# Performance work log

Measured on AMD Instinct MI355X. Metric: run time of the kernel, lower is better.

## Reference

```python
import jax, jax.numpy as jnp
import numpy as np

S, D, BN, GH, AH, FCH = 18, 512, 32, 128, 16, 512


def setup_inputs() -> dict:
    key = jax.random.key(0)
    ks = jax.random.split(key, 20)
    B = 8192
    sc = 0.05
    inp = {
        "local_styles": jax.random.normal(ks[0], (B, S, D), jnp.float32),
        "global_styles": jax.random.normal(ks[1], (B, S, D), jnp.float32),
        "target_ages": jax.random.uniform(ks[2], (B,), jnp.float32),
        # per-style bottleneck MLPs (512->32->32), stacked over styles
        "bn_w1": jax.random.normal(ks[3], (S, D, BN), jnp.float32) * sc,
        "bn_b1": jnp.zeros((S, BN), jnp.float32),
        "bn_w2": jax.random.normal(ks[4], (S, BN, BN), jnp.float32) * sc,
        "bn_b2": jnp.zeros((S, BN), jnp.float32),
        # global mlp (18*32 -> 128 -> 128)
        "gm_w1": jax.random.normal(ks[5], (S * BN, GH), jnp.float32) * sc,
        "gm_b1": jnp.zeros((GH,), jnp.float32),
        "gm_w2": jax.random.normal(ks[6], (GH, GH), jnp.float32) * sc,
        "gm_b2": jnp.zeros((GH,), jnp.float32),
        # age mlp (1 -> 16 -> 16)
        "age_w1": jax.random.normal(ks[7], (1, AH), jnp.float32) * sc,
        "age_b1": jnp.zeros((AH,), jnp.float32),
        "age_w2": jax.random.normal(ks[8], (AH, AH), jnp.float32) * sc,
        "age_b2": jnp.zeros((AH,), jnp.float32),
        # per-style fc MLPs (128+16+512 -> 512 -> 512), stacked over styles
        "fc_w1": jax.random.normal(ks[9], (S, GH + AH + D, FCH), jnp.float32) * sc,
        "fc_b1": jnp.zeros((S, FCH), jnp.float32),
        "fc_w2": jax.random.normal(ks[10], (S, FCH, D), jnp.float32) * sc,
        "fc_b2": jnp.zeros((S, D), jnp.float32),
    }
    return inp


def reference(local_styles, global_styles, target_ages,
              bn_w1, bn_b1, bn_w2, bn_b2,
              gm_w1, gm_b1, gm_w2, gm_b2,
              age_w1, age_b1, age_w2, age_b2,
              fc_w1, fc_b1, fc_w2, fc_b2):
    B = global_styles.shape[0]
    # per-style bottlenecks as batched GEMMs over the style axis
    h = jax.nn.relu(jnp.einsum('bsd,sdk->bsk', global_styles, bn_w1) + bn_b1)
    h = jnp.einsum('bsk,skm->bsm', h, bn_w2) + bn_b2          # [B, S, 32]
    gf = h.reshape(B, S * BN)                                  # concat over styles
    gf = jax.nn.relu(gf @ gm_w1 + gm_b1) @ gm_w2 + gm_b2      # [B, 128]
    af = target_ages[:, None]                                  # [B, 1]
    af = jax.nn.relu(af @ age_w1 + age_b1) @ age_w2 + age_b2   # [B, 16]
    gfa = jnp.concatenate([gf, af], axis=1)                    # [B, 144]
    # per-style fc: input is [global_feats, style_i] -> [B, S, 656]
    x = jnp.concatenate([jnp.broadcast_to(gfa[:, None, :], (B, S, GH + AH)),
                         global_styles], axis=2)
    y = jax.nn.relu(jnp.einsum('bsf,sfh->bsh', x, fc_w1) + fc_b1)
    y = jnp.einsum('bsh,shd->bsd', y, fc_w2) + fc_b2
    return y + global_styles
```

## Files before the change

kernel.cpp:

```cpp
#include <hip/hip_runtime.h>

typedef unsigned short u16;
typedef unsigned int   u32;
typedef __attribute__((ext_vector_type(4))) float floatx4;
typedef __attribute__((ext_vector_type(8))) short shortx8;

#define BB 8192
#define SS 18
#define DD 512

__device__ __forceinline__ u16 f2bf(float f){
  u32 u = __float_as_uint(f);
  return (u16)((u + 0x7FFFu + ((u >> 16) & 1u)) >> 16);
}

__device__ __forceinline__ shortx8 pack8v(floatx4 a, floatx4 b){
  shortx8 t;
  t[0]=(short)f2bf(a[0]); t[1]=(short)f2bf(a[1]); t[2]=(short)f2bf(a[2]); t[3]=(short)f2bf(a[3]);
  t[4]=(short)f2bf(b[0]); t[5]=(short)f2bf(b[1]); t[6]=(short)f2bf(b[2]); t[7]=(short)f2bf(b[3]);
  return t;
}

__device__ __forceinline__ void gload16(const void* g, void* l){
  __builtin_amdgcn_global_load_lds((const __attribute__((address_space(1))) void*)g,
                                   (__attribute__((address_space(3))) void*)l, 16, 0, 0);
}

template<int CALLS>
__device__ __forceinline__ void gstage(const char* src, size_t rowStrideB, int chunkByteOff,
                                       char* lds, int wid, int lane){
#pragma unroll
  for (int i=0;i<CALLS;++i){
    int base = (wid*CALLS + i)*1024;
    int off  = base + lane*16;
    int row  = off >> 7;
    int blk  = ((off >> 4) & 7) ^ (row & 7);
    gload16(src + (size_t)row*rowStrideB + chunkByteOff + blk*16, lds + base);
  }
}

__device__ __forceinline__ void lds_store4(char* buf, int row, int rowBytes, int khByte,
                                           int swzMask, const shortx8* v){
#pragma unroll
  for (int q=0;q<4;++q){
    int off = row*rowBytes + khByte + q*16;
    off ^= (row & swzMask) << 4;
    *(shortx8*)(buf + off) = v[q];
  }
}

__device__ __forceinline__ void stage_bf16(char* buf, const u16* gsrc, size_t srcRowBytes, int tid){
  int row = tid >> 1, kh = tid & 1;
  const char* p = (const char*)gsrc + (size_t)row*srcRowBytes + kh*64;
  shortx8 v[4];
#pragma unroll
  for (int q=0;q<4;++q) v[q] = *(const shortx8*)(p + q*16);
  lds_store4(buf, row, 128, kh*64, 7, v);
}

__device__ __forceinline__ shortx8 lds_frag(const char* buf, int row, int rowBytes, int kByte,
                                            int swzMask, int lane){
  int off = row*rowBytes + kByte + ((lane>>4)<<4);
  off ^= (row & swzMask) << 4;
  return *(const shortx8*)(buf + off);
}

template<int MF, int NF>
__device__ __forceinline__ void mma64(const char* As, const char* Bs, int wm, int wn, int lane,
                                      floatx4 acc[MF][NF]){
#pragma unroll
  for (int kk=0; kk<2; ++kk){
    shortx8 a[MF], b[NF];
#pragma unroll
    for (int i=0;i<MF;++i) a[i] = lds_frag(As, wm + i*16 + (lane&15), 128, kk*64, 7, lane);
#pragma unroll
    for (int j=0;j<NF;++j) b[j] = lds_frag(Bs, wn + j*16 + (lane&15), 128, kk*64, 7, lane);
#pragma unroll
    for (int i=0;i<MF;++i)
#pragma unroll
      for (int j=0;j<NF;++j)
        acc[i][j] = __builtin_amdgcn_mfma_f32_16x16x32_bf16(a[i], b[j], acc[i][j], 0, 0, 0);
  }
}

__device__ __forceinline__ int xcd_swz(int bid, int nwg){
  int q = nwg >> 3;
  return (bid & 7)*q + (bid >> 3);
}

__global__ __launch_bounds__(256) void transpose_w2(const float* __restrict__ src,
                                                    u16* __restrict__ dst,
                                                    int sKstride, int kSrcOff, int Kuse,
                                                    int N, int Kpad, int kDstOff){
  __shared__ float tile[32][33];
  int s = blockIdx.z;
  int k0 = blockIdx.x*32, n0 = blockIdx.y*32;
  int tx = threadIdx.x & 31, ty = threadIdx.x >> 5;
#pragma unroll
  for (int r=0;r<4;++r){
    int k = k0 + ty*4 + r;
    float v = (k < Kuse) ? src[((size_t)s*sKstride + kSrcOff + k)*N + n0 + tx] : 0.f;
    tile[ty*4+r][tx] = v;
  }
  __syncthreads();
#pragma unroll
  for (int r=0;r<4;++r){
    int n = n0 + ty*4 + r;
    dst[((size_t)s*N + n)*Kpad + kDstOff + k0 + tx] = f2bf(tile[tx][ty*4+r]);
  }
}

__global__ __launch_bounds__(256) void k_bn(const float* __restrict__ gs,
     const u16* __restrict__ w1t, const u16* __restrict__ w2t,
     const float* __restrict__ b1, const float* __restrict__ b2,
     u16* __restrict__ h2b){
  __shared__ __align__(16) char SMB[40960];
  int tid = threadIdx.x, lane = tid & 63, wid = tid >> 6;
  int nb = xcd_swz(blockIdx.x, 1152);
  int m0 = (nb & 63)*128, s = nb >> 6;
  floatx4 acc[2][2] = {};
  const char*  Bsrc = (const char*)w1t + (size_t)s*32*1024;
  const float* Ags  = gs + ((size_t)(m0 + (tid>>1))*SS + s)*DD + (tid&1)*32;
  floatx4 fr[8];
  gstage<1>((const char*)Bsrc, 1024, 0, SMB+32768, wid, lane);
#pragma unroll
  for (int q=0;q<8;++q) fr[q] = *(const floatx4*)(Ags + q*4);
  for (int c=0;c<8;++c){
    char* Asc = SMB + (c&1)*16384;
    char* Bsc = SMB + 32768 + (c&1)*4096;
    { shortx8 v[4];
#pragma unroll
      for (int q=0;q<4;++q) v[q] = pack8v(fr[2*q], fr[2*q+1]);
      lds_store4(Asc, tid>>1, 128, (tid&1)*64, 7, v); }
    __syncthreads();
    int cn = c+1;
    if (cn < 8){
      gstage<1>(Bsrc, 1024, cn*128, SMB + 32768 + (cn&1)*4096, wid, lane);
      const float* p = Ags + cn*64;
#pragma unroll
      for (int q=0;q<8;++q) fr[q] = *(const floatx4*)(p + q*4);
    }
    mma64<2,2>(Asc, Bsc, wid*32, 0, lane, acc);
  }
  __syncthreads();
  char* G1  = SMB;
  char* W2s = SMB + 8192;
#pragma unroll
  for (int i=0;i<2;++i)
#pragma unroll
   for (int j=0;j<2;++j){
    int col = j*16 + (lane&15);
    float bias = b1[s*32 + col];
#pragma unroll
    for (int r=0;r<4;++r){
      int row = wid*32 + i*16 + ((lane>>4)<<2) + r;
      float v = fmaxf(acc[i][j][r] + bias, 0.f);
      int off = (row*64 + col*2) ^ ((row&3)<<4);
      *(u16*)(G1 + off) = f2bf(v);
    }
  }
  if (tid < 32){
    const u16* p = w2t + (size_t)s*32*32 + tid*32;
#pragma unroll
    for (int q=0;q<4;++q){
      int off = (tid*64 + q*16) ^ ((tid&3)<<4);
      *(shortx8*)(W2s + off) = *(const shortx8*)(p + q*8);
    }
  }
  __syncthreads();
  floatx4 acc2[2][2] = {};
  {
    shortx8 a[2], b[2];
#pragma unroll
    for (int i=0;i<2;++i) a[i] = lds_frag(G1,  wid*32 + i*16 + (lane&15), 64, 0, 3, lane);
#pragma unroll
    for (int j=0;j<2;++j) b[j] = lds_frag(W2s, j*16 + (lane&15),          64, 0, 3, lane);
#pragma unroll
    for (int i=0;i<2;++i)
#pragma unroll
      for (int j=0;j<2;++j)
        acc2[i][j] = __builtin_amdgcn_mfma_f32_16x16x32_bf16(a[i], b[j], acc2[i][j], 0,0,0);
  }
#pragma unroll
  for (int i=0;i<2;++i)
#pragma unroll
   for (int j=0;j<2;++j){
    int col = j*16 + (lane&15);
    float bias = b2[s*32 + col];
#pragma unroll
    for (int r=0;r<4;++r){
      int row = wid*32 + i*16 + ((lane>>4)<<2) + r;
      h2b[((size_t)(m0+row)*SS + s)*32 + col] = f2bf(acc2[i][j][r] + bias);
    }
  }
}

__global__ __launch_bounds__(256) void k_gm(const u16* __restrict__ h2b,
     const u16* __restrict__ w1t, const u16* __restrict__ w2t,
     const float* __restrict__ b1, const float* __restrict__ b2,
     const float* __restrict__ ta, const float* __restrict__ aw1, const float* __restrict__ ab1,
     const float* __restrict__ aw2, const float* __restrict__ ab2,
     u16* __restrict__ gfab){
  __shared__ __align__(16) char As[128*128];
  __shared__ __align__(16) char Bs[128*128];
  __shared__ __align__(16) char G1[128*256];
  int tid=threadIdx.x, lane=tid&63, w=tid>>6;
  int m0 = blockIdx.x*128;
  floatx4 acc[2][8] = {};
  for (int c=0;c<9;++c){
    __syncthreads();
    stage_bf16(As, h2b + (size_t)m0*576 + c*64, 1152, tid);
    stage_bf16(Bs, w1t + c*64,                 1152, tid);
    __syncthreads();
    mma64<2,8>(As, Bs, w*32, 0, lane, acc);
  }
#pragma unroll
  for (int i=0;i<2;++i)
#pragma unroll
   for (int j=0;j<8;++j){
    int col = j*16 + (lane&15);
    float bias = b1[col];
#pragma unroll
    for (int r=0;r<4;++r){
      int row = w*32 + i*16 + ((lane>>4)<<2) + r;
      float v = fmaxf(acc[i][j][r] + bias, 0.f);
      int off = (row*256 + col*2) ^ ((row&7)<<4);
      *(u16*)(G1 + off) = f2bf(v);
    }
  }
  floatx4 acc2[2][8] = {};
  for (int c2=0;c2<2;++c2){
    __syncthreads();
    stage_bf16(Bs, w2t + c2*64, 256, tid);
    __syncthreads();
#pragma unroll
    for (int kk=0;kk<2;++kk){
      shortx8 a[2], b[8];
#pragma unroll
      for (int i=0;i<2;++i){
        int row = w*32 + i*16 + (lane&15);
        int off = (row*256 + c2*128 + kk*64 + ((lane>>4)<<4)) ^ ((row&7)<<4);
        a[i] = *(const shortx8*)(G1 + off);
      }
#pragma unroll
      for (int j=0;j<8;++j) b[j] = lds_frag(Bs, j*16 + (lane&15), 128, kk*64, 7, lane);
#pragma unroll
      for (int i=0;i<2;++i)
#pragma unroll
        for (int j=0;j<8;++j)
          acc2[i][j] = __builtin_amdgcn_mfma_f32_16x16x32_bf16(a[i], b[j], acc2[i][j], 0,0,0);
    }
  }
#pragma unroll
  for (int i=0;i<2;++i)
#pragma unroll
   for (int j=0;j<8;++j){
    int col = j*16 + (lane&15);
    float bias = b2[col];
#pragma unroll
    for (int r=0;r<4;++r){
      int row = w*32 + i*16 + ((lane>>4)<<2) + r;
      gfab[(size_t)(m0+row)*192 + col] = f2bf(acc2[i][j][r] + bias);
    }
  }
  if (tid < 128){
    int bidx = m0 + tid;
    float t = ta[bidx];
    float a1[16];
#pragma unroll
    for (int j2=0;j2<16;++j2){ float v = t*aw1[j2] + ab1[j2]; a1[j2] = fmaxf(v, 0.f); }
#pragma unroll
    for (int m=0;m<16;++m){
      float v = ab2[m];
#pragma unroll
      for (int j2=0;j2<16;++j2) v += a1[j2]*aw2[j2*16+m];
      gfab[(size_t)bidx*192 + 128 + m] = f2bf(v);
    }
    shortx8 zz = {};
#pragma unroll
    for (int z=0;z<6;++z) *(shortx8*)(gfab + (size_t)bidx*192 + 144 + z*8) = zz;
  }
}

__global__ __launch_bounds__(256) void k_fc1(const u16* __restrict__ gfab,
     const float* __restrict__ gs, const u16* __restrict__ w1t,
     const float* __restrict__ b1, u16* __restrict__ y1b){
  __shared__ __align__(16) char SMB[65536];
  int tid=threadIdx.x, lane=tid&63, wid=tid>>6;
  int nb = xcd_swz(blockIdx.x, 4608);
  int n0 = (nb&3)*128, m0 = ((nb>>2)&63)*128, s = nb>>8;
  int wm=(wid>>1)*64, wn=(wid&1)*64;
  floatx4 acc[4][4] = {};
  const char*  Asrc0 = (const char*)gfab + (size_t)m0*384;
  const char*  Bsrc  = (const char*)w1t + ((size_t)s*512 + n0)*1408;
  const float* Ags   = gs + ((size_t)(m0 + (tid>>1))*SS + s)*DD + (tid&1)*32;
  floatx4 fr[8];
  gstage<4>(Asrc0, 384, 0, SMB, wid, lane);
  gstage<4>(Bsrc, 1408, 0, SMB+32768, wid, lane);
  for (int c=0;c<11;++c){
    char* Asc = SMB + (c&1)*16384;
    char* Bsc = SMB + 32768 + (c&1)*16384;
    if (c >= 3){
      shortx8 v[4];
#pragma unroll
      for (int q=0;q<4;++q) v[q] = pack8v(fr[2*q], fr[2*q+1]);
      lds_store4(Asc, tid>>1, 128, (tid&1)*64, 7, v);
    }
    __syncthreads();
    int cn = c+1;
    if (cn < 11){
      gstage<4>(Bsrc, 1408, cn*128, SMB + 32768 + (cn&1)*16384, wid, lane);
      if (cn < 3){
        gstage<4>(Asrc0, 384, cn*128, SMB + (cn&1)*16384, wid, lane);
      } else {
        const float* p = Ags + (cn*64 - 192);
#pragma unroll
        for (int q=0;q<8;++q) fr[q] = *(const floatx4*)(p + q*4);
      }
    }
    mma64<4,4>(Asc, Bsc, wm, wn, lane, acc);
  }
  __syncthreads();
  char* OT = SMB;
#pragma unroll
  for (int i=0;i<4;++i)
#pragma unroll
   for (int j=0;j<4;++j){
    int col = wn + j*16 + (lane&15);
    float bias = b1[(size_t)s*512 + n0 + col];
#pragma unroll
    for (int r=0;r<4;++r){
      int row = wm + i*16 + ((lane>>4)<<2) + r;
      float v = fmaxf(acc[i][j][r] + bias, 0.f);
      int off = (row*256 + col*2) ^ ((row&7)<<4);
      *(u16*)(OT + off) = f2bf(v);
    }
  }
  __syncthreads();
  {
    int row = tid>>1, half = tid&1;
    u16* gp = y1b + ((size_t)(m0+row)*SS + s)*DD + n0 + half*64;
#pragma unroll
    for (int q=0;q<8;++q){
      int off = (row*256 + half*128 + q*16) ^ ((row&7)<<4);
      *(shortx8*)(gp + q*8) = *(const shortx8*)(OT + off);
    }
  }
}

__global__ __launch_bounds__(256) void k_fc2(const u16* __restrict__ y1b,
     const float* __restrict__ gs, const u16* __restrict__ w2t,
     const float* __restrict__ b2, float* __restrict__ out){
  __shared__ __align__(16) char SMB[65536];
  int tid=threadIdx.x, lane=tid&63, wid=tid>>6;
  int nb = xcd_swz(blockIdx.x, 4608);
  int n0 = (nb&3)*128, m0 = ((nb>>2)&63)*128, s = nb>>8;
  int wm=(wid>>1)*64, wn=(wid&1)*64;
  floatx4 acc[4][4] = {};
  const char* Asrc = (const char*)y1b + ((size_t)m0*SS + s)*1024;
  const char* Bsrc = (const char*)w2t + ((size_t)s*512 + n0)*1024;
  gstage<4>(Asrc, (size_t)SS*1024, 0, SMB, wid, lane);
  gstage<4>(Bsrc, 1024, 0, SMB+32768, wid, lane);
  for (int c=0;c<8;++c){
    char* Asc = SMB + (c&1)*16384;
    char* Bsc = SMB + 32768 + (c&1)*16384;
    __syncthreads();
    int cn = c+1;
    if (cn < 8){
      gstage<4>(Asrc, (size_t)SS*1024, cn*128, SMB + (cn&1)*16384, wid, lane);
      gstage<4>(Bsrc, 1024, cn*128, SMB + 32768 + (cn&1)*16384, wid, lane);
    }
    mma64<4,4>(Asc, Bsc, wm, wn, lane, acc);
  }
  __syncthreads();
  float* SMF = (float*)SMB;
#pragma unroll
  for (int i=0;i<4;++i)
#pragma unroll
   for (int j=0;j<4;++j){
    int col = wn + j*16 + (lane&15);
#pragma unroll
    for (int r=0;r<4;++r){
      int row = wm + i*16 + ((lane>>4)<<2) + r;
      int off = (row*512 + col*4) ^ ((row&7)<<4);
      *(float*)((char*)SMF + off) = acc[i][j][r];
    }
  }
  __syncthreads();
  {
    int row = tid>>1, half = tid&1;
    size_t gidx = ((size_t)(m0+row)*SS + s)*DD + n0 + half*64;
    const float* bp = b2 + (size_t)s*512 + n0 + half*64;
#pragma unroll
    for (int q=0;q<16;++q){
      int off = (row*512 + half*256 + q*16) ^ ((row&7)<<4);
      floatx4 v = *(const floatx4*)((const char*)SMF + off);
      floatx4 g = *(const floatx4*)(gs + gidx + q*4);
      floatx4 bb = *(const floatx4*)(bp + q*4);
      *(floatx4*)(out + gidx + q*4) = v + g + bb;
    }
  }
}

extern "C" void kernel_launch(void* const* d_in, const int* in_sizes, int n_in,
                              void* d_out, int out_size, void* d_ws, size_t ws_size,
                              hipStream_t stream){
  (void)in_sizes; (void)n_in; (void)out_size; (void)ws_size;
  const float* gs   = (const float*)d_in[1];
  const float* ta   = (const float*)d_in[2];
  const float* bnw1 = (const float*)d_in[3];
  const float* bnb1 = (const float*)d_in[4];
  const float* bnw2 = (const float*)d_in[5];
  const float* bnb2 = (const float*)d_in[6];
  const float* gmw1 = (const float*)d_in[7];
  const float* gmb1 = (const float*)d_in[8];
  const float* gmw2 = (const float*)d_in[9];
  const float* gmb2 = (const float*)d_in[10];
  const float* aw1  = (const float*)d_in[11];
  const float* ab1  = (const float*)d_in[12];
  const float* aw2  = (const float*)d_in[13];
  const float* ab2  = (const float*)d_in[14];
  const float* fcw1 = (const float*)d_in[15];
  const float* fcb1 = (const float*)d_in[16];
  const float* fcw2 = (const float*)d_in[17];
  const float* fcb2 = (const float*)d_in[18];

  char* ws = (char*)d_ws;
  u16* fcW1t = (u16*)(ws + 0);
  u16* fcW2t = (u16*)(ws + 12976128);
  u16* bnW1t = (u16*)(ws + 22413312);
  u16* bnW2t = (u16*)(ws + 23003136);
  u16* gmW1t = (u16*)(ws + 23040000);
  u16* gmW2t = (u16*)(ws + 23187456);
  u16* h2b   = (u16*)(ws + 23220224);
  u16* gfab  = (u16*)(ws + 32657408);
  u16* y1b   = (u16*)(ws + 35803136);
  float* out = (float*)d_out;

  dim3 blk(256);
  transpose_w2<<<dim3(16,1,18),  blk, 0, stream>>>(bnw1, bnW1t, 512, 0, 512,  32, 512, 0);
  transpose_w2<<<dim3(1,1,18),   blk, 0, stream>>>(bnw2, bnW2t,  32, 0,  32,  32,  32, 0);
  transpose_w2<<<dim3(18,4,1),   blk, 0, stream>>>(gmw1, gmW1t, 576, 0, 576, 128, 576, 0);
  transpose_w2<<<dim3(4,4,1),    blk, 0, stream>>>(gmw2, gmW2t, 128, 0, 128, 128, 128, 0);
  transpose_w2<<<dim3(6,16,18),  blk, 0, stream>>>(fcw1, fcW1t, 656, 0,   144, 512, 704, 0);
  transpose_w2<<<dim3(16,16,18), blk, 0, stream>>>(fcw1, fcW1t, 656, 144, 512, 512, 704, 192);
  transpose_w2<<<dim3(16,16,18), blk, 0, stream>>>(fcw2, fcW2t, 512, 0, 512, 512, 512, 0);

  k_bn <<<dim3(1152), blk, 0, stream>>>(gs, bnW1t, bnW2t, bnb1, bnb2, h2b);
  k_gm <<<dim3(64),   blk, 0, stream>>>(h2b, gmW1t, gmW2t, gmb1, gmb2, ta, aw1, ab1, aw2, ab2, gfab);
  k_fc1<<<dim3(4608), blk, 0, stream>>>(gfab, gs, fcW1t, fcb1, y1b);
  k_fc2<<<dim3(4608), blk, 0, stream>>>(y1b, gs, fcW2t, fcb2, out);
}
```

Before: 687.1 us.

## Cache bf16 copy of global_styles and deepen fc GEMM pipelines with async loads

```diff
diff --git a/kernel.cpp b/kernel.cpp
--- a/kernel.cpp
+++ b/kernel.cpp
@@ -13,6 +13,7 @@
   u32 u = __float_as_uint(f);
   return (u16)((u + 0x7FFFu + ((u >> 16) & 1u)) >> 16);
 }
+__device__ __forceinline__ float bf2f(u16 x){ return __uint_as_float(((u32)x)<<16); }
 
 __device__ __forceinline__ shortx8 pack8v(floatx4 a, floatx4 b){
   shortx8 t;
@@ -81,6 +82,28 @@
       for (int j=0;j<NF;++j)
         acc[i][j] = __builtin_amdgcn_mfma_f32_16x16x32_bf16(a[i], b[j], acc[i][j], 0, 0, 0);
   }
+}
+
+template<int MF, int NF>
+__device__ __forceinline__ void frags_load(const char* As, const char* Bs, int wm, int wn, int lane,
+                                           shortx8 a[2][MF], shortx8 b[2][NF]){
+#pragma unroll
+  for (int kk=0;kk<2;++kk){
+#pragma unroll
+    for (int i=0;i<MF;++i) a[kk][i] = lds_frag(As, wm + i*16 + (lane&15), 128, kk*64, 7, lane);
+#pragma unroll
+    for (int j=0;j<NF;++j) b[kk][j] = lds_frag(Bs, wn + j*16 + (lane&15), 128, kk*64, 7, lane);
+  }
+}
+template<int MF, int NF>
+__device__ __forceinline__ void frags_mma(shortx8 a[2][MF], shortx8 b[2][NF], floatx4 acc[MF][NF]){
+#pragma unroll
+  for (int kk=0;kk<2;++kk)
+#pragma unroll
+    for (int i=0;i<MF;++i)
+#pragma unroll
+      for (int j=0;j<NF;++j)
+        acc[i][j] = __builtin_amdgcn_mfma_f32_16x16x32_bf16(a[kk][i], b[kk][j], acc[i][j], 0, 0, 0);
 }
 
 __device__ __forceinline__ int xcd_swz(int bid, int nwg){
@@ -113,16 +136,18 @@
 __global__ __launch_bounds__(256) void k_bn(const float* __restrict__ gs,
      const u16* __restrict__ w1t, const u16* __restrict__ w2t,
      const float* __restrict__ b1, const float* __restrict__ b2,
-     u16* __restrict__ h2b){
+     u16* __restrict__ h2b, u16* __restrict__ gsb){
   __shared__ __align__(16) char SMB[40960];
   int tid = threadIdx.x, lane = tid & 63, wid = tid >> 6;
   int nb = xcd_swz(blockIdx.x, 1152);
   int m0 = (nb & 63)*128, s = nb >> 6;
   floatx4 acc[2][2] = {};
   const char*  Bsrc = (const char*)w1t + (size_t)s*32*1024;
-  const float* Ags  = gs + ((size_t)(m0 + (tid>>1))*SS + s)*DD + (tid&1)*32;
+  size_t rowIdx = ((size_t)(m0 + (tid>>1))*SS + s)*DD + (tid&1)*32;
+  const float* Ags  = gs + rowIdx;
+  u16*         Gsb  = gsb + rowIdx;
   floatx4 fr[8];
-  gstage<1>((const char*)Bsrc, 1024, 0, SMB+32768, wid, lane);
+  gstage<1>(Bsrc, 1024, 0, SMB+32768, wid, lane);
 #pragma unroll
   for (int q=0;q<8;++q) fr[q] = *(const floatx4*)(Ags + q*4);
   for (int c=0;c<8;++c){
@@ -131,6 +156,9 @@
     { shortx8 v[4];
 #pragma unroll
       for (int q=0;q<4;++q) v[q] = pack8v(fr[2*q], fr[2*q+1]);
+      u16* gp = Gsb + c*64;
+#pragma unroll
+      for (int q=0;q<4;++q) *(shortx8*)(gp + q*8) = v[q];
       lds_store4(Asc, tid>>1, 128, (tid&1)*64, 7, v); }
     __syncthreads();
     int cn = c+1;
@@ -283,42 +311,33 @@
 }
 
 __global__ __launch_bounds__(256) void k_fc1(const u16* __restrict__ gfab,
-     const float* __restrict__ gs, const u16* __restrict__ w1t,
+     const u16* __restrict__ gsb, const u16* __restrict__ w1t,
      const float* __restrict__ b1, u16* __restrict__ y1b){
-  __shared__ __align__(16) char SMB[65536];
+  __shared__ __align__(16) char SMB[81920];
   int tid=threadIdx.x, lane=tid&63, wid=tid>>6;
   int nb = xcd_swz(blockIdx.x, 4608);
-  int n0 = (nb&3)*128, m0 = ((nb>>2)&63)*128, s = nb>>8;
+  int n0=(nb&3)*128, m0=((nb>>2)&63)*128, s=nb>>8;
   int wm=(wid>>1)*64, wn=(wid&1)*64;
   floatx4 acc[4][4] = {};
-  const char*  Asrc0 = (const char*)gfab + (size_t)m0*384;
-  const char*  Bsrc  = (const char*)w1t + ((size_t)s*512 + n0)*1408;
-  const float* Ags   = gs + ((size_t)(m0 + (tid>>1))*SS + s)*DD + (tid&1)*32;
-  floatx4 fr[8];
-  gstage<4>(Asrc0, 384, 0, SMB, wid, lane);
-  gstage<4>(Bsrc, 1408, 0, SMB+32768, wid, lane);
+  const char* Ag   = (const char*)gfab + (size_t)m0*384;
+  const char* Agl  = (const char*)gsb + ((size_t)m0*SS + s)*1024;
+  const char* Bsrc = (const char*)w1t + ((size_t)s*512+n0)*1408;
+#define F1_ISSA(t) do{ int _t=(t); char* _d = SMB + (_t%3)*16384; \
+    if (_t<3) gstage<4>(Ag, 384, _t*128, _d, wid, lane); \
+    else      gstage<4>(Agl, (size_t)SS*1024, _t*128-384, _d, wid, lane); }while(0)
+#define F1_ISSB(t) gstage<4>(Bsrc, 1408, (t)*128, SMB+49152+((t)&1)*16384, wid, lane)
+  F1_ISSB(0); F1_ISSA(0); F1_ISSA(1);
+#pragma unroll 1
   for (int c=0;c<11;++c){
-    char* Asc = SMB + (c&1)*16384;
-    char* Bsc = SMB + 32768 + (c&1)*16384;
-    if (c >= 3){
-      shortx8 v[4];
-#pragma unroll
-      for (int q=0;q<4;++q) v[q] = pack8v(fr[2*q], fr[2*q+1]);
-      lds_store4(Asc, tid>>1, 128, (tid&1)*64, 7, v);
-    }
-    __syncthreads();
-    int cn = c+1;
-    if (cn < 11){
-      gstage<4>(Bsrc, 1408, cn*128, SMB + 32768 + (cn&1)*16384, wid, lane);
-      if (cn < 3){
-        gstage<4>(Asrc0, 384, cn*128, SMB + (cn&1)*16384, wid, lane);
-      } else {
-        const float* p = Ags + (cn*64 - 192);
-#pragma unroll
-        for (int q=0;q<8;++q) fr[q] = *(const floatx4*)(p + q*4);
-      }
-    }
-    mma64<4,4>(Asc, Bsc, wm, wn, lane, acc);
+    if (c<10) asm volatile("s_waitcnt vmcnt(4)" ::: "memory");
+    else      asm volatile("s_waitcnt vmcnt(0)" ::: "memory");
+    __builtin_amdgcn_s_barrier();
+    __builtin_amdgcn_sched_barrier(0);
+    shortx8 a[2][4], b[2][4];
+    frags_load<4,4>(SMB+(c%3)*16384, SMB+49152+(c&1)*16384, wm, wn, lane, a, b);
+    if (c+1<11) F1_ISSB(c+1);
+    if (c+2<11) F1_ISSA(c+2);
+    frags_mma<4,4>(a, b, acc);
   }
   __syncthreads();
   char* OT = SMB;
@@ -349,28 +368,30 @@
 }
 
 __global__ __launch_bounds__(256) void k_fc2(const u16* __restrict__ y1b,
-     const float* __restrict__ gs, const u16* __restrict__ w2t,
+     const u16* __restrict__ gsb, const u16* __restrict__ w2t,
      const float* __restrict__ b2, float* __restrict__ out){
-  __shared__ __align__(16) char SMB[65536];
+  __shared__ __align__(16) char SMB[81920];
   int tid=threadIdx.x, lane=tid&63, wid=tid>>6;
   int nb = xcd_swz(blockIdx.x, 4608);
-  int n0 = (nb&3)*128, m0 = ((nb>>2)&63)*128, s = nb>>8;
+  int n0=(nb&3)*128, m0=((nb>>2)&63)*128, s=nb>>8;
   int wm=(wid>>1)*64, wn=(wid&1)*64;
   floatx4 acc[4][4] = {};
   const char* Asrc = (const char*)y1b + ((size_t)m0*SS + s)*1024;
   const char* Bsrc = (const char*)w2t + ((size_t)s*512 + n0)*1024;
-  gstage<4>(Asrc, (size_t)SS*1024, 0, SMB, wid, lane);
-  gstage<4>(Bsrc, 1024, 0, SMB+32768, wid, lane);
+#define F2_ISSA(t) gstage<4>(Asrc, (size_t)SS*1024, (t)*128, SMB+((t)%3)*16384, wid, lane)
+#define F2_ISSB(t) gstage<4>(Bsrc, 1024, (t)*128, SMB+49152+((t)&1)*16384, wid, lane)
+  F2_ISSB(0); F2_ISSA(0); F2_ISSA(1);
+#pragma unroll 1
   for (int c=0;c<8;++c){
-    char* Asc = SMB + (c&1)*16384;
-    char* Bsc = SMB + 32768 + (c&1)*16384;
-    __syncthreads();
-    int cn = c+1;
-    if (cn < 8){
-      gstage<4>(Asrc, (size_t)SS*1024, cn*128, SMB + (cn&1)*16384, wid, lane);
-      gstage<4>(Bsrc, 1024, cn*128, SMB + 32768 + (cn&1)*16384, wid, lane);
-    }
-    mma64<4,4>(Asc, Bsc, wm, wn, lane, acc);
+    if (c<7) asm volatile("s_waitcnt vmcnt(4)" ::: "memory");
+    else     asm volatile("s_waitcnt vmcnt(0)" ::: "memory");
+    __builtin_amdgcn_s_barrier();
+    __builtin_amdgcn_sched_barrier(0);
+    shortx8 a[2][4], b[2][4];
+    frags_load<4,4>(SMB+(c%3)*16384, SMB+49152+(c&1)*16384, wm, wn, lane, a, b);
+    if (c+1<8) F2_ISSB(c+1);
+    if (c+2<8) F2_ISSA(c+2);
+    frags_mma<4,4>(a, b, acc);
   }
   __syncthreads();
   float* SMF = (float*)SMB;
@@ -391,13 +412,21 @@
     int row = tid>>1, half = tid&1;
     size_t gidx = ((size_t)(m0+row)*SS + s)*DD + n0 + half*64;
     const float* bp = b2 + (size_t)s*512 + n0 + half*64;
-#pragma unroll
-    for (int q=0;q<16;++q){
-      int off = (row*512 + half*256 + q*16) ^ ((row&7)<<4);
-      floatx4 v = *(const floatx4*)((const char*)SMF + off);
-      floatx4 g = *(const floatx4*)(gs + gidx + q*4);
-      floatx4 bb = *(const floatx4*)(bp + q*4);
-      *(floatx4*)(out + gidx + q*4) = v + g + bb;
+    const u16*   gp = gsb + gidx;
+#pragma unroll
+    for (int q2=0;q2<8;++q2){
+      shortx8 gv = *(const shortx8*)(gp + q2*8);
+      int off0 = (row*512 + half*256 + (2*q2)*16)   ^ ((row&7)<<4);
+      int off1 = (row*512 + half*256 + (2*q2+1)*16) ^ ((row&7)<<4);
+      floatx4 v0 = *(const floatx4*)((char*)SMF + off0);
+      floatx4 v1 = *(const floatx4*)((char*)SMF + off1);
+      floatx4 b0 = *(const floatx4*)(bp + q2*8);
+      floatx4 b1v= *(const floatx4*)(bp + q2*8 + 4);
+      floatx4 g0, g1;
+      g0[0]=bf2f((u16)gv[0]); g0[1]=bf2f((u16)gv[1]); g0[2]=bf2f((u16)gv[2]); g0[3]=bf2f((u16)gv[3]);
+      g1[0]=bf2f((u16)gv[4]); g1[1]=bf2f((u16)gv[5]); g1[2]=bf2f((u16)gv[6]); g1[3]=bf2f((u16)gv[7]);
+      *(floatx4*)(out + gidx + q2*8)     = v0 + b0 + g0;
+      *(floatx4*)(out + gidx + q2*8 + 4) = v1 + b1v + g1;
     }
   }
 }
@@ -435,6 +464,7 @@
   u16* h2b   = (u16*)(ws + 23220224);
   u16* gfab  = (u16*)(ws + 32657408);
   u16* y1b   = (u16*)(ws + 35803136);
+  u16* gsb   = (u16*)(ws + 186798080);
   float* out = (float*)d_out;
 
   dim3 blk(256);
@@ -446,8 +476,8 @@
   transpose_w2<<<dim3(16,16,18), blk, 0, stream>>>(fcw1, fcW1t, 656, 144, 512, 512, 704, 192);
   transpose_w2<<<dim3(16,16,18), blk, 0, stream>>>(fcw2, fcW2t, 512, 0, 512, 512, 512, 0);
 
-  k_bn <<<dim3(1152), blk, 0, stream>>>(gs, bnW1t, bnW2t, bnb1, bnb2, h2b);
+  k_bn <<<dim3(1152), blk, 0, stream>>>(gs, bnW1t, bnW2t, bnb1, bnb2, h2b, gsb);
   k_gm <<<dim3(64),   blk, 0, stream>>>(h2b, gmW1t, gmW2t, gmb1, gmb2, ta, aw1, ab1, aw2, ab2, gfab);
-  k_fc1<<<dim3(4608), blk, 0, stream>>>(gfab, gs, fcW1t, fcb1, y1b);
-  k_fc2<<<dim3(4608), blk, 0, stream>>>(y1b, gs, fcW2t, fcb2, out);
-}
+  k_fc1<<<dim3(4608), blk, 0, stream>>>(gfab, gsb, fcW1t, fcb1, y1b);
+  k_fc2<<<dim3(4608), blk, 0, stream>>>(y1b, gsb, fcW2t, fcb2, out);
+}
```

Measured after the change: 573.4 us. 1.2x faster.

## Restructure fc GEMMs with a bf16 style copy, register A-loads, and a 3-stage B pipeline

Applied to the files above, without the earlier changes.

```diff
diff --git a/kernel.cpp b/kernel.cpp
--- a/kernel.cpp
+++ b/kernel.cpp
@@ -13,6 +13,7 @@
   u32 u = __float_as_uint(f);
   return (u16)((u + 0x7FFFu + ((u >> 16) & 1u)) >> 16);
 }
+__device__ __forceinline__ float bf2f(u16 x){ return __uint_as_float(((u32)x)<<16); }
 
 __device__ __forceinline__ shortx8 pack8v(floatx4 a, floatx4 b){
   shortx8 t;
@@ -32,6 +33,18 @@
 #pragma unroll
   for (int i=0;i<CALLS;++i){
     int base = (wid*CALLS + i)*1024;
+    int off  = base + lane*16;
+    int row  = off >> 7;
+    int blk  = ((off >> 4) & 7) ^ (row & 7);
+    gload16(src + (size_t)row*rowStrideB + chunkByteOff + blk*16, lds + base);
+  }
+}
+
+__device__ __forceinline__ void gstage8(const char* src, size_t rowStrideB, int chunkByteOff,
+                                        char* lds, int wid, int lane){
+#pragma unroll
+  for (int i=0;i<2;++i){
+    int base = (wid*2 + i)*1024;
     int off  = base + lane*16;
     int row  = off >> 7;
     int blk  = ((off >> 4) & 7) ^ (row & 7);
@@ -113,7 +126,7 @@
 __global__ __launch_bounds__(256) void k_bn(const float* __restrict__ gs,
      const u16* __restrict__ w1t, const u16* __restrict__ w2t,
      const float* __restrict__ b1, const float* __restrict__ b2,
-     u16* __restrict__ h2b){
+     u16* __restrict__ h2b, u16* __restrict__ gsb){
   __shared__ __align__(16) char SMB[40960];
   int tid = threadIdx.x, lane = tid & 63, wid = tid >> 6;
   int nb = xcd_swz(blockIdx.x, 1152);
@@ -121,8 +134,9 @@
   floatx4 acc[2][2] = {};
   const char*  Bsrc = (const char*)w1t + (size_t)s*32*1024;
   const float* Ags  = gs + ((size_t)(m0 + (tid>>1))*SS + s)*DD + (tid&1)*32;
+  u16*         Gsb  = gsb + ((size_t)s*BB + m0 + (tid>>1))*DD + (tid&1)*32;
   floatx4 fr[8];
-  gstage<1>((const char*)Bsrc, 1024, 0, SMB+32768, wid, lane);
+  gstage<1>(Bsrc, 1024, 0, SMB+32768, wid, lane);
 #pragma unroll
   for (int q=0;q<8;++q) fr[q] = *(const floatx4*)(Ags + q*4);
   for (int c=0;c<8;++c){
@@ -131,6 +145,9 @@
     { shortx8 v[4];
 #pragma unroll
       for (int q=0;q<4;++q) v[q] = pack8v(fr[2*q], fr[2*q+1]);
+      u16* gp = Gsb + c*64;
+#pragma unroll
+      for (int q=0;q<4;++q) *(shortx8*)(gp + q*8) = v[q];
       lds_store4(Asc, tid>>1, 128, (tid&1)*64, 7, v); }
     __syncthreads();
     int cn = c+1;
@@ -282,122 +299,178 @@
   }
 }
 
-__global__ __launch_bounds__(256) void k_fc1(const u16* __restrict__ gfab,
-     const float* __restrict__ gs, const u16* __restrict__ w1t,
+__global__ __launch_bounds__(512, 4) void k_fc1(const u16* __restrict__ gfab,
+     const u16* __restrict__ gsb, const u16* __restrict__ w1t,
      const float* __restrict__ b1, u16* __restrict__ y1b){
-  __shared__ __align__(16) char SMB[65536];
+  __shared__ __align__(16) char SMB[49152];
   int tid=threadIdx.x, lane=tid&63, wid=tid>>6;
   int nb = xcd_swz(blockIdx.x, 4608);
-  int n0 = (nb&3)*128, m0 = ((nb>>2)&63)*128, s = nb>>8;
-  int wm=(wid>>1)*64, wn=(wid&1)*64;
-  floatx4 acc[4][4] = {};
-  const char*  Asrc0 = (const char*)gfab + (size_t)m0*384;
-  const char*  Bsrc  = (const char*)w1t + ((size_t)s*512 + n0)*1408;
-  const float* Ags   = gs + ((size_t)(m0 + (tid>>1))*SS + s)*DD + (tid&1)*32;
-  floatx4 fr[8];
-  gstage<4>(Asrc0, 384, 0, SMB, wid, lane);
-  gstage<4>(Bsrc, 1408, 0, SMB+32768, wid, lane);
+  int n2 = nb&3, m0 = ((nb>>2)&63)*128, s = nb>>8;
+  int wm = (wid&3)*32, wn = (wid>>2)*64;
+  floatx4 acc[2][4] = {};
+  const char* pAg[2]; const char* pAs[2];
+#pragma unroll
+  for (int i=0;i<2;++i){
+    int r = m0 + wm + 16*i + (lane&15);
+    pAg[i] = (const char*)gfab + (size_t)r*384 + ((lane>>4)<<4);
+    pAs[i] = (const char*)gsb + ((size_t)s*BB + r)*1024 + ((lane>>4)<<4);
+  }
+  const char* gW = (const char*)w1t + ((size_t)s*512 + n2*128)*1408;
+  shortx8 aA[2][2], aB[2][2];
+#define LDA1(tc, A) do{ \
+    if ((tc) < 3){ \
+      A[0][0]=*(const shortx8*)(pAg[0]+(tc)*128);    A[0][1]=*(const shortx8*)(pAg[1]+(tc)*128); \
+      A[1][0]=*(const shortx8*)(pAg[0]+(tc)*128+64); A[1][1]=*(const shortx8*)(pAg[1]+(tc)*128+64); \
+    } else { \
+      A[0][0]=*(const shortx8*)(pAs[0]+((tc)-3)*128);    A[0][1]=*(const shortx8*)(pAs[1]+((tc)-3)*128); \
+      A[1][0]=*(const shortx8*)(pAs[0]+((tc)-3)*128+64); A[1][1]=*(const shortx8*)(pAs[1]+((tc)-3)*128+64); \
+    } }while(0)
+#define CHUNK1(c, ACUR, ANXT) do{ \
+    if ((c)<10) asm volatile("s_waitcnt vmcnt(2)" ::: "memory"); \
+    else        asm volatile("s_waitcnt vmcnt(0)" ::: "memory"); \
+    __builtin_amdgcn_s_barrier(); \
+    __builtin_amdgcn_sched_barrier(0); \
+    if ((c)+1<11) LDA1((c)+1, ANXT); \
+    __builtin_amdgcn_sched_barrier(0); \
+    if ((c)+2<11) gstage8(gW, 1408, ((c)+2)*128, SMB + (((c)+2)%3)*16384, wid, lane); \
+    __builtin_amdgcn_sched_barrier(0); \
+    const char* Bb = SMB + ((c)%3)*16384; \
+    _Pragma("unroll") \
+    for (int kk=0;kk<2;++kk){ \
+      shortx8 b[4]; \
+      _Pragma("unroll") \
+      for (int j=0;j<4;++j) b[j] = lds_frag(Bb, wn + j*16 + (lane&15), 128, kk*64, 7, lane); \
+      __builtin_amdgcn_s_setprio(1); \
+      _Pragma("unroll") \
+      for (int i=0;i<2;++i) \
+        _Pragma("unroll") \
+        for (int j=0;j<4;++j) \
+          acc[i][j] = __builtin_amdgcn_mfma_f32_16x16x32_bf16(ACUR[kk][i], b[j], acc[i][j], 0,0,0); \
+      __builtin_amdgcn_s_setprio(0); \
+    } }while(0)
+  LDA1(0, aA);
+  gstage8(gW, 1408, 0, SMB, wid, lane);
+  gstage8(gW, 1408, 128, SMB+16384, wid, lane);
+#pragma unroll
   for (int c=0;c<11;++c){
-    char* Asc = SMB + (c&1)*16384;
-    char* Bsc = SMB + 32768 + (c&1)*16384;
-    if (c >= 3){
-      shortx8 v[4];
-#pragma unroll
-      for (int q=0;q<4;++q) v[q] = pack8v(fr[2*q], fr[2*q+1]);
-      lds_store4(Asc, tid>>1, 128, (tid&1)*64, 7, v);
-    }
-    __syncthreads();
-    int cn = c+1;
-    if (cn < 11){
-      gstage<4>(Bsrc, 1408, cn*128, SMB + 32768 + (cn&1)*16384, wid, lane);
-      if (cn < 3){
-        gstage<4>(Asrc0, 384, cn*128, SMB + (cn&1)*16384, wid, lane);
-      } else {
-        const float* p = Ags + (cn*64 - 192);
-#pragma unroll
-        for (int q=0;q<8;++q) fr[q] = *(const floatx4*)(p + q*4);
-      }
-    }
-    mma64<4,4>(Asc, Bsc, wm, wn, lane, acc);
+    if (c&1) CHUNK1(c, aB, aA); else CHUNK1(c, aA, aB);
   }
   __syncthreads();
-  char* OT = SMB;
-#pragma unroll
-  for (int i=0;i<4;++i)
+#pragma unroll
+  for (int i=0;i<2;++i)
 #pragma unroll
    for (int j=0;j<4;++j){
     int col = wn + j*16 + (lane&15);
-    float bias = b1[(size_t)s*512 + n0 + col];
+    float bias = b1[(size_t)s*512 + n2*128 + col];
 #pragma unroll
     for (int r=0;r<4;++r){
       int row = wm + i*16 + ((lane>>4)<<2) + r;
       float v = fmaxf(acc[i][j][r] + bias, 0.f);
       int off = (row*256 + col*2) ^ ((row&7)<<4);
-      *(u16*)(OT + off) = f2bf(v);
+      *(u16*)(SMB + off) = f2bf(v);
     }
   }
   __syncthreads();
   {
-    int row = tid>>1, half = tid&1;
-    u16* gp = y1b + ((size_t)(m0+row)*SS + s)*DD + n0 + half*64;
-#pragma unroll
-    for (int q=0;q<8;++q){
-      int off = (row*256 + half*128 + q*16) ^ ((row&7)<<4);
-      *(shortx8*)(gp + q*8) = *(const shortx8*)(OT + off);
-    }
-  }
-}
-
-__global__ __launch_bounds__(256) void k_fc2(const u16* __restrict__ y1b,
-     const float* __restrict__ gs, const u16* __restrict__ w2t,
+    int row = tid>>2, q4 = tid&3;
+    u16* gp = y1b + ((size_t)s*BB + m0 + row)*DD + n2*128 + q4*32;
+#pragma unroll
+    for (int q=0;q<4;++q){
+      int off = (row*256 + q4*64 + q*16) ^ ((row&7)<<4);
+      *(shortx8*)(gp + q*8) = *(const shortx8*)(SMB + off);
+    }
+  }
+}
+
+__global__ __launch_bounds__(512, 4) void k_fc2(const u16* __restrict__ y1b,
+     const u16* __restrict__ gsb, const u16* __restrict__ w2t,
      const float* __restrict__ b2, float* __restrict__ out){
-  __shared__ __align__(16) char SMB[65536];
+  __shared__ __align__(16) char SMB[49152];
   int tid=threadIdx.x, lane=tid&63, wid=tid>>6;
   int nb = xcd_swz(blockIdx.x, 4608);
-  int n0 = (nb&3)*128, m0 = ((nb>>2)&63)*128, s = nb>>8;
-  int wm=(wid>>1)*64, wn=(wid&1)*64;
-  floatx4 acc[4][4] = {};
-  const char* Asrc = (const char*)y1b + ((size_t)m0*SS + s)*1024;
-  const char* Bsrc = (const char*)w2t + ((size_t)s*512 + n0)*1024;
-  gstage<4>(Asrc, (size_t)SS*1024, 0, SMB, wid, lane);
-  gstage<4>(Bsrc, 1024, 0, SMB+32768, wid, lane);
+  int n2 = nb&3, m0 = ((nb>>2)&63)*128, s = nb>>8;
+  int wm = (wid&3)*32, wn = (wid>>2)*64;
+  floatx4 acc[2][4] = {};
+  const char* pA[2];
+#pragma unroll
+  for (int i=0;i<2;++i){
+    int r = m0 + wm + 16*i + (lane&15);
+    pA[i] = (const char*)y1b + ((size_t)s*BB + r)*1024 + ((lane>>4)<<4);
+  }
+  const char* gW = (const char*)w2t + ((size_t)s*512 + n2*128)*1024;
+  shortx8 aA[2][2], aB[2][2];
+#define LDA2(tc, A) do{ \
+    A[0][0]=*(const shortx8*)(pA[0]+(tc)*128);    A[0][1]=*(const shortx8*)(pA[1]+(tc)*128); \
+    A[1][0]=*(const shortx8*)(pA[0]+(tc)*128+64); A[1][1]=*(const shortx8*)(pA[1]+(tc)*128+64); \
+  }while(0)
+#define CHUNK2(c, ACUR, ANXT) do{ \
+    if ((c)<7) asm volatile("s_waitcnt vmcnt(2)" ::: "memory"); \
+    else       asm volatile("s_waitcnt vmcnt(0)" ::: "memory"); \
+    __builtin_amdgcn_s_barrier(); \
+    __builtin_amdgcn_sched_barrier(0); \
+    if ((c)+1<8) LDA2((c)+1, ANXT); \
+    __builtin_amdgcn_sched_barrier(0); \
+    if ((c)+2<8) gstage8(gW, 1024, ((c)+2)*128, SMB + (((c)+2)%3)*16384, wid, lane); \
+    __builtin_amdgcn_sched_barrier(0); \
+    const char* Bb = SMB + ((c)%3)*16384; \
+    _Pragma("unroll") \
+    for (int kk=0;kk<2;++kk){ \
+      shortx8 b[4]; \
+      _Pragma("unroll") \
+      for (int j=0;j<4;++j) b[j] = lds_frag(Bb, wn + j*16 + (lane&15), 128, kk*64, 7, lane); \
+      __builtin_amdgcn_s_setprio(1); \
+      _Pragma("unroll") \
+      for (int i=0;i<2;++i) \
+        _Pragma("unroll") \
+        for (int j=0;j<4;++j) \
+          acc[i][j] = __builtin_amdgcn_mfma_f32_16x16x32_bf16(ACUR[kk][i], b[j], acc[i][j], 0,0,0); \
+      __builtin_amdgcn_s_setprio(0); \
+    } }while(0)
+  LDA2(0, aA);
+  gstage8(gW, 1024, 0, SMB, wid, lane);
+  gstage8(gW, 1024, 128, SMB+16384, wid, lane);
+#pragma unroll
   for (int c=0;c<8;++c){
-    char* Asc = SMB + (c&1)*16384;
-    char* Bsc = SMB + 32768 + (c&1)*16384;
-    __syncthreads();
-    int cn = c+1;
-    if (cn < 8){
-      gstage<4>(Asrc, (size_t)SS*1024, cn*128, SMB + (cn&1)*16384, wid, lane);
-      gstage<4>(Bsrc, 1024, cn*128, SMB + 32768 + (cn&1)*16384, wid, lane);
-    }
-    mma64<4,4>(Asc, Bsc, wm, wn, lane, acc);
-  }
-  __syncthreads();
+    if (c&1) CHUNK2(c, aB, aA); else CHUNK2(c, aA, aB);
+  }
   float* SMF = (float*)SMB;
-#pragma unroll
-  for (int i=0;i<4;++i)
-#pragma unroll
-   for (int j=0;j<4;++j){
-    int col = wn + j*16 + (lane&15);
-#pragma unroll
-    for (int r=0;r<4;++r){
-      int row = wm + i*16 + ((lane>>4)<<2) + r;
-      int off = (row*512 + col*4) ^ ((row&7)<<4);
-      *(float*)((char*)SMF + off) = acc[i][j][r];
-    }
-  }
-  __syncthreads();
-  {
-    int row = tid>>1, half = tid&1;
-    size_t gidx = ((size_t)(m0+row)*SS + s)*DD + n0 + half*64;
-    const float* bp = b2 + (size_t)s*512 + n0 + half*64;
-#pragma unroll
-    for (int q=0;q<16;++q){
-      int off = (row*512 + half*256 + q*16) ^ ((row&7)<<4);
-      floatx4 v = *(const floatx4*)((const char*)SMF + off);
-      floatx4 g = *(const floatx4*)(gs + gidx + q*4);
-      floatx4 bb = *(const floatx4*)(bp + q*4);
-      *(floatx4*)(out + gidx + q*4) = v + g + bb;
+#pragma unroll 1
+  for (int h=0;h<2;++h){
+    __syncthreads();
+    if (((wid&3)>>1) == h){
+#pragma unroll
+      for (int i=0;i<2;++i)
+#pragma unroll
+       for (int j=0;j<4;++j){
+        int col = wn + j*16 + (lane&15);
+#pragma unroll
+        for (int r=0;r<4;++r){
+          int rl = ((wid&1)*32) + i*16 + ((lane>>4)<<2) + r;
+          int off = (rl*512 + col*4) ^ ((rl&7)<<4);
+          *(float*)((char*)SMF + off) = acc[i][j][r];
+        }
+      }
+    }
+    __syncthreads();
+    {
+      int rl = tid>>3, e8 = tid&7;
+      int grow = m0 + h*64 + rl;
+      size_t gidx = ((size_t)grow*SS + s)*DD + n2*128 + e8*16;
+      const float* bp = b2 + (size_t)s*512 + n2*128 + e8*16;
+      const u16*   gp = gsb + ((size_t)s*BB + grow)*DD + n2*128 + e8*16;
+      shortx8 gv[2];
+      gv[0] = *(const shortx8*)(gp);
+      gv[1] = *(const shortx8*)(gp + 8);
+#pragma unroll
+      for (int q=0;q<4;++q){
+        int off = (rl*512 + e8*64 + q*16) ^ ((rl&7)<<4);
+        floatx4 v = *(const floatx4*)((char*)SMF + off);
+        floatx4 bb = *(const floatx4*)(bp + q*4);
+        floatx4 g;
+        g[0]=bf2f((u16)gv[q>>1][(q&1)*4+0]); g[1]=bf2f((u16)gv[q>>1][(q&1)*4+1]);
+        g[2]=bf2f((u16)gv[q>>1][(q&1)*4+2]); g[3]=bf2f((u16)gv[q>>1][(q&1)*4+3]);
+        *(floatx4*)(out + gidx + q*4) = v + bb + g;
+      }
     }
   }
 }
@@ -435,6 +508,7 @@
   u16* h2b   = (u16*)(ws + 23220224);
   u16* gfab  = (u16*)(ws + 32657408);
   u16* y1b   = (u16*)(ws + 35803136);
+  u16* gsb   = (u16*)(ws + 186798080);
   float* out = (float*)d_out;
 
   dim3 blk(256);
@@ -446,8 +520,8 @@
   transpose_w2<<<dim3(16,16,18), blk, 0, stream>>>(fcw1, fcW1t, 656, 144, 512, 512, 704, 192);
   transpose_w2<<<dim3(16,16,18), blk, 0, stream>>>(fcw2, fcW2t, 512, 0, 512, 512, 512, 0);
 
-  k_bn <<<dim3(1152), blk, 0, stream>>>(gs, bnW1t, bnW2t, bnb1, bnb2, h2b);
-  k_gm <<<dim3(64),   blk, 0, stream>>>(h2b, gmW1t, gmW2t, gmb1, gmb2, ta, aw1, ab1, aw2, ab2, gfab);
-  k_fc1<<<dim3(4608), blk, 0, stream>>>(gfab, gs, fcW1t, fcb1, y1b);
-  k_fc2<<<dim3(4608), blk, 0, stream>>>(y1b, gs, fcW2t, fcb2, out);
-}
+  k_bn <<<dim3(1152), blk,       0, stream>>>(gs, bnW1t, bnW2t, bnb1, bnb2, h2b, gsb);
+  k_gm <<<dim3(64),   blk,       0, stream>>>(h2b, gmW1t, gmW2t, gmb1, gmb2, ta, aw1, ab1, aw2, ab2, gfab);
+  k_fc1<<<dim3(4608), dim3(512), 0, stream>>>(gfab, gsb, fcW1t, fcb1, y1b);
+  k_fc2<<<dim3(4608), dim3(512), 0, stream>>>(y1b, gsb, fcW2t, fcb2, out);
+}
```

New measurement: 720.8 us. 4.9% more time.
